# Optimization experiments

Measured on AMD Instinct MI355X. Metric: run time of the kernel, lower is better.

The kernel has to match this reference:

```python
import jax, jax.numpy as jnp
import numpy as np
from jax import lax

N, D = 8, 32            # batch, map_depth
S = 2                   # belief_downsample_factor
HS, WS = 512, 512       # semantic map resolution
H, W = HS // S, WS // S # belief resolution (256, 256)
K = 7                   # motion_kernel_size
KK = K * K
HID = 64                # motion_hidden_size
A = 256                 # action_embedding_size


def _conv(x, w, b, pad, dil=1):
    # x: NCHW, w: OIHW
    y = lax.conv_general_dilated(
        x, w, window_strides=(1, 1), padding=[(pad, pad), (pad, pad)],
        rhs_dilation=(dil, dil), dimension_numbers=('NCHW', 'OIHW', 'NCHW'))
    return y + b[None, :, None, None]


def _unfold_index():
    # Reproduces nn.Unfold([K,K]) applied to ConstantPad2d(K//2, -1)(arange image).
    # Result flattened in (ki*K+kj, i, j) order, matching col2im flatten order.
    pad = K // 2
    img = np.arange(H * W, dtype=np.int64).reshape(H, W)
    imgp = np.pad(img, ((pad, pad), (pad, pad)), constant_values=-1)
    idx = np.empty((K, K, H, W), dtype=np.int64)
    for ki in range(K):
        for kj in range(K):
            idx[ki, kj] = imgp[ki:ki + H, kj:kj + W]
    return idx.reshape(-1)  # (K*K*H*W,)

_IDX = _unfold_index()
_VALID = _IDX >= 0
_IDX_SAFE = np.where(_VALID, _IDX, 0)


def _scatter_logsumexp(src, idx, num_segments):
    # src: (B, M) with -inf marking invalid entries; idx: (M,) shared across B.
    def one(s):
        mx = jax.ops.segment_max(s, idx, num_segments=num_segments)          # (P,)
        g = mx[idx]                                                          # (M,)
        contrib = jnp.where(jnp.isneginf(s), 0.0,
                            jnp.exp(s - jnp.where(jnp.isfinite(g), g, 0.0)))
        sm = jax.ops.segment_sum(contrib, idx, num_segments=num_segments)    # (P,)
        return mx + jnp.log(jnp.where(jnp.isfinite(mx), sm, 1.0))
    return jax.vmap(one)(src)


def setup_inputs() -> dict:
    key = jax.random.key(0)
    ks = jax.random.split(key, 20)
    f32 = jnp.float32
    return {
        'log_belief': jax.random.normal(ks[0], (N, 1, H, W), f32),
        'semantic_map': jax.random.normal(ks[1], (N, D, HS, WS), f32),
        'action': jax.random.normal(ks[2], (N, A), f32),
        # Bottleneck(map_depth -> hidden -> map_depth, dilations [3,1])
        'w_in': jax.random.normal(ks[3], (HID, D, 1, 1), f32) * 0.1,
        'b_in': jnp.zeros((HID,), f32),
        'w_d3': jax.random.normal(ks[4], (HID, HID, 3, 3), f32) * 0.05,
        'b_d3': jnp.zeros((HID,), f32),
        'w_d1': jax.random.normal(ks[5], (HID, HID, 3, 3), f32) * 0.05,
        'b_d1': jnp.zeros((HID,), f32),
        'w_out': jax.random.normal(ks[6], (D, HID, 1, 1), f32) * 0.1,
        'b_out': jnp.zeros((D,), f32),
        # conv1x1: map_depth -> K*K
        'w_k': jax.random.normal(ks[7], (KK, D, 1, 1), f32) * 0.1,
        'b_k': jnp.zeros((KK,), f32),
        # DenseMlpBlock2: A -> hidden -> K*K
        'w_a1': jax.random.normal(ks[8], (A, HID), f32) * 0.05,
        'b_a1': jnp.zeros((HID,), f32),
        'w_a2': jax.random.normal(ks[9], (HID, KK), f32) * 0.05,
        'b_a2': jnp.zeros((KK,), f32),
    }


def reference(log_belief, semantic_map, action,
              w_in, b_in, w_d3, b_d3, w_d1, b_d1, w_out, b_out,
              w_k, b_k, w_a1, b_a1, w_a2, b_a2):
    # Dropout in eval mode -> identity. MaxPool2d(S, stride=S):
    x = lax.reduce_window(semantic_map, -jnp.inf, lax.max,
                          (1, 1, S, S), (1, 1, S, S), 'VALID')  # (N,D,H,W)
    # Bottleneck (conv1x1 -> dilated 3x3 convs -> conv1x1, residual)
    h = jax.nn.relu(_conv(x, w_in, b_in, 0))
    h = jax.nn.relu(_conv(h, w_d3, b_d3, 3, 3))
    h = jax.nn.relu(_conv(h, w_d1, b_d1, 1, 1))
    x2 = x + _conv(h, w_out, b_out, 0)
    # motion kernel logits over K*K taps per pixel
    motion = jax.nn.log_softmax(_conv(x2, w_k, b_k, 0), axis=1)   # (N,KK,H,W)
    lang = jax.nn.log_softmax(
        jax.nn.relu(action @ w_a1 + b_a1) @ w_a2 + b_a2, axis=1)  # (N,KK)
    log_kernel = jax.nn.log_softmax(motion + lang[:, :, None, None], axis=1)
    # propagate_belief: col2im + scatter_logsumexp (C=1, Cin=Cout=1)
    src = (log_belief + log_kernel).reshape(N, -1)                # (N, KK*H*W)
    idx = jnp.asarray(_IDX_SAFE)
    src = jnp.where(jnp.asarray(_VALID)[None, :], src, -jnp.inf)
    new_belief = _scatter_logsumexp(src, idx, H * W)              # (N, H*W)
    return new_belief.reshape(N, 1, H, W)
```

## Files before the change

kernel.cpp:

```cpp
#include <hip/hip_runtime.h>
#include <hip/hip_bf16.h>

typedef __hip_bfloat16 bf16;
typedef __attribute__((ext_vector_type(8)))  short  short8;
typedef __attribute__((ext_vector_type(16))) float  floatx16;

#define HW 65536

__device__ __forceinline__ float b2f(bf16 v){ return __bfloat162float(v); }
__device__ __forceinline__ bf16  f2b(float v){ return __float2bfloat16(v); }
__device__ __forceinline__ unsigned short f2bu(float v){
  union { bf16 h; unsigned short u; } cv; cv.h = __float2bfloat16(v); return cv.u;
}
__device__ __forceinline__ float bu2f(unsigned short u){
  union { unsigned u; float f; } cv; cv.u = ((unsigned)u) << 16; return cv.f;
}

__global__ void prep_w33(const float* __restrict__ w, bf16* __restrict__ wb){
  int i = blockIdx.x*256 + threadIdx.x;
  if (i >= 36864) return;
  int j    = i & 7;
  int gran = i >> 3;
  int oc   = gran & 63;
  int rest = gran >> 6;
  int half = rest & 1;
  int ks   = (rest >> 1) & 3;
  int t    = rest >> 3;
  int e  = ks*16 + half*8 + j;
  int ki = t / 3, kj = t - ki*3;
  wb[i] = f2b(w[(oc*64 + e)*9 + ki*3 + kj]);
}

__global__ void lang_kernel(const float* __restrict__ action,
                            const float* __restrict__ w_a1, const float* __restrict__ b_a1,
                            const float* __restrict__ w_a2, const float* __restrict__ b_a2,
                            float* __restrict__ lang){
  int n = blockIdx.x; int t = threadIdx.x;
  __shared__ float hid[64];
  __shared__ float logits[49];
  __shared__ float lse_sh;
  float acc = b_a1[t];
  for (int a = 0; a < 256; a++) acc += action[n*256+a] * w_a1[a*64+t];
  hid[t] = fmaxf(acc, 0.f);
  __syncthreads();
  if (t < 49){
    float l = b_a2[t];
    for (int j = 0; j < 64; j++) l += hid[j] * w_a2[j*49+t];
    logits[t] = l;
  }
  __syncthreads();
  if (t == 0){
    float m = -1e30f;
    for (int k = 0; k < 49; k++) m = fmaxf(m, logits[k]);
    float s = 0.f;
    for (int k = 0; k < 49; k++) s += __expf(logits[k]-m);
    lse_sh = m + __logf(s);
  }
  __syncthreads();
  if (t < 49) lang[n*49+t] = logits[t] - lse_sh;
}

__global__ __launch_bounds__(256) void pool_in_kernel(
    const float* __restrict__ sm, const float* __restrict__ w_in,
    const float* __restrict__ b_in, float* __restrict__ x, bf16* __restrict__ h1){
  int p = blockIdx.x*256 + threadIdx.x;
  int n = p >> 16; int ij = p & 65535; int i = ij >> 8; int j = ij & 255;
  const float* smn = sm + ((long)n << 23);
  float xv[32];
  #pragma unroll
  for (int d = 0; d < 32; d++){
    long base = ((long)(d*512 + 2*i) << 9) + 2*j;
    float2 p0 = *reinterpret_cast<const float2*>(smn + base);
    float2 p1 = *reinterpret_cast<const float2*>(smn + base + 512);
    xv[d] = fmaxf(fmaxf(p0.x, p0.y), fmaxf(p1.x, p1.y));
  }
  float4* xo = reinterpret_cast<float4*>(x + ((long)p << 5));
  #pragma unroll
  for (int q = 0; q < 8; q++)
    xo[q] = make_float4(xv[4*q], xv[4*q+1], xv[4*q+2], xv[4*q+3]);
  unsigned ow[32];
  #pragma unroll 4
  for (int c = 0; c < 64; c += 2){
    float a0 = b_in[c], a1 = b_in[c+1];
    #pragma unroll
    for (int d = 0; d < 32; d++){
      a0 += xv[d]*w_in[c*32+d];
      a1 += xv[d]*w_in[(c+1)*32+d];
    }
    ow[c>>1] = ((unsigned)f2bu(fmaxf(a1,0.f)) << 16) | f2bu(fmaxf(a0,0.f));
  }
  uint4* ho = reinterpret_cast<uint4*>((char*)h1 + ((long)p << 7));
  #pragma unroll
  for (int q = 0; q < 8; q++)
    ho[q] = make_uint4(ow[4*q], ow[4*q+1], ow[4*q+2], ow[4*q+3]);
}

template<int DIL>
__global__ __launch_bounds__(256) void conv3x3_mfma(
    const bf16* __restrict__ hin, const bf16* __restrict__ wb,
    const float* __restrict__ bias, bf16* __restrict__ hout){
  constexpr int R = 16 + 2*DIL, C = 16 + 2*DIL, NPIX = R*C;
  __shared__ __align__(16) char tile[NPIX*128];
  int b = blockIdx.x;
  int n = b >> 8; int tb = b & 255;
  int i0 = (tb >> 4) << 4, j0 = (tb & 15) << 4;
  int tid = threadIdx.x;
  const bf16* hn = hin + ((long)n << 22);
  for (int s = tid; s < NPIX*8; s += 256){
    int pix = s >> 3, g = s & 7;
    int r = pix / C, c = pix - r*C;
    int gi = i0 - DIL + r, gj = j0 - DIL + c;
    uint4 v = make_uint4(0u,0u,0u,0u);
    if (gi >= 0 && gi < 256 && gj >= 0 && gj < 256)
      v = *reinterpret_cast<const uint4*>(hn + (((long)((gi<<8) + gj)) << 6) + (g<<3));
    *reinterpret_cast<uint4*>(tile + pix*128 + ((g ^ (pix & 7)) << 4)) = v;
  }
  __syncthreads();
  int lane = tid & 63, wv = tid >> 6;
  int mg = wv >> 1, nt = wv & 1;
  int l31 = lane & 31, half = lane >> 5;
  floatx16 acc[4];
  #pragma unroll
  for (int mt = 0; mt < 4; mt++) acc[mt] = (floatx16)(0.0f);
  int prr[4], pcc[4];
  #pragma unroll
  for (int mt = 0; mt < 4; mt++){
    int pidx = (mg*4 + mt)*32 + l31;
    prr[mt] = pidx >> 4; pcc[mt] = pidx & 15;
  }
  const char* wbc = reinterpret_cast<const char*>(wb);
  for (int t = 0; t < 9; t++){
    int ki = t / 3, kj = t - ki*3;
    int pp[4];
    #pragma unroll
    for (int mt = 0; mt < 4; mt++)
      pp[mt] = (prr[mt] + ki*DIL)*C + (pcc[mt] + kj*DIL);
    #pragma unroll
    for (int ks = 0; ks < 4; ks++){
      short8 bfrag = *reinterpret_cast<const short8*>(
          wbc + ((((t*4 + ks)*2 + half)*64 + nt*32 + l31) << 4));
      #pragma unroll
      for (int mt = 0; mt < 4; mt++){
        short8 afrag = *reinterpret_cast<const short8*>(
            tile + pp[mt]*128 + (((ks*2 + half) ^ (pp[mt] & 7)) << 4));
        acc[mt] = __builtin_amdgcn_mfma_f32_32x32x16_bf16(afrag, bfrag, acc[mt], 0, 0, 0);
      }
    }
  }
  float bv = bias[nt*32 + l31];
  bf16* ho = hout + ((long)n << 22);
  #pragma unroll
  for (int mt = 0; mt < 4; mt++){
    #pragma unroll
    for (int reg = 0; reg < 16; reg++){
      int row = (reg & 3) + 8*(reg >> 2) + 4*half;
      int pidx = (mg*4 + mt)*32 + row;
      int pr = pidx >> 4, pc = pidx & 15;
      ho[(((long)(((i0+pr)<<8) + (j0+pc))) << 6) + nt*32 + l31] =
          f2b(fmaxf(acc[mt][reg] + bv, 0.f));
    }
  }
}

__global__ __launch_bounds__(256) void out_motion_kernel(
    const bf16* __restrict__ h3, const float* __restrict__ x,
    const float* __restrict__ w_out, const float* __restrict__ b_out,
    const float* __restrict__ w_k, const float* __restrict__ b_k,
    const float* __restrict__ lang, float* __restrict__ lk){
  int p = blockIdx.x*256 + threadIdx.x;
  int n = p >> 16; int ij = p & 65535;
  float hv[64];
  const uint4* hp = reinterpret_cast<const uint4*>((const char*)h3 + ((long)p << 7));
  #pragma unroll
  for (int q = 0; q < 8; q++){
    uint4 u = hp[q];
    unsigned uu[4] = {u.x, u.y, u.z, u.w};
    #pragma unroll
    for (int k = 0; k < 4; k++){
      hv[q*8 + 2*k]   = bu2f((unsigned short)(uu[k] & 0xffffu));
      hv[q*8 + 2*k+1] = bu2f((unsigned short)(uu[k] >> 16));
    }
  }
  float o[32];
  const float4* xp = reinterpret_cast<const float4*>(x + ((long)p << 5));
  #pragma unroll
  for (int q = 0; q < 8; q++){
    float4 tq = xp[q];
    o[4*q] = tq.x; o[4*q+1] = tq.y; o[4*q+2] = tq.z; o[4*q+3] = tq.w;
  }
  #pragma unroll 4
  for (int d = 0; d < 32; d++){
    float acc = b_out[d];
    #pragma unroll
    for (int e = 0; e < 64; e++) acc += hv[e]*w_out[d*64+e];
    o[d] += acc;
  }
  float lg[49]; float m = -1e30f;
  #pragma unroll 7
  for (int k = 0; k < 49; k++){
    float acc = b_k[k] + lang[n*49+k];
    #pragma unroll
    for (int d = 0; d < 32; d++) acc += o[d]*w_k[k*32+d];
    lg[k] = acc; m = fmaxf(m, acc);
  }
  float s = 0.f;
  #pragma unroll
  for (int k = 0; k < 49; k++) s += __expf(lg[k]-m);
  float lse = m + __logf(s);
  #pragma unroll
  for (int k = 0; k < 49; k++) lk[(long)n*49*HW + (long)k*HW + ij] = lg[k] - lse;
}

__global__ __launch_bounds__(256) void gather_lse_kernel(
    const float* __restrict__ lb, const float* __restrict__ lk, float* __restrict__ out){
  int p = blockIdx.x*256 + threadIdx.x;
  int n = p >> 16; int ij = p & 65535; int i = ij >> 8; int j = ij & 255;
  const float* lkn = lk + (long)n*49*HW;
  float v[49]; float m = -1e30f;
  #pragma unroll
  for (int ki = 0; ki < 7; ki++){
    int h = i + 3 - ki;
    bool hok = (h >= 0 && h < 256);
    #pragma unroll
    for (int kj = 0; kj < 7; kj++){
      int w = j + 3 - kj;
      float val = -1e30f;
      if (hok && w >= 0 && w < 256){
        int q = h*256 + w;
        val = lb[n*HW + q] + lkn[(ki*7+kj)*HW + q];
      }
      v[ki*7+kj] = val; m = fmaxf(m, val);
    }
  }
  float s = 0.f;
  #pragma unroll
  for (int t = 0; t < 49; t++) s += __expf(v[t]-m);
  out[p] = m + __logf(s);
}

extern "C" void kernel_launch(void* const* d_in, const int* in_sizes, int n_in,
                              void* d_out, int out_size, void* d_ws, size_t ws_size,
                              hipStream_t stream) {
  (void)in_sizes; (void)n_in; (void)out_size; (void)ws_size;
  const float* lb    = (const float*)d_in[0];
  const float* sm    = (const float*)d_in[1];
  const float* act   = (const float*)d_in[2];
  const float* w_in  = (const float*)d_in[3];
  const float* b_in  = (const float*)d_in[4];
  const float* w_d3  = (const float*)d_in[5];
  const float* b_d3  = (const float*)d_in[6];
  const float* w_d1  = (const float*)d_in[7];
  const float* b_d1  = (const float*)d_in[8];
  const float* w_out = (const float*)d_in[9];
  const float* b_out = (const float*)d_in[10];
  const float* w_k   = (const float*)d_in[11];
  const float* b_k   = (const float*)d_in[12];
  const float* w_a1  = (const float*)d_in[13];
  const float* b_a1  = (const float*)d_in[14];
  const float* w_a2  = (const float*)d_in[15];
  const float* b_a2  = (const float*)d_in[16];
  float* out = (float*)d_out;

  char* ws = (char*)d_ws;
  float* x    = (float*)(ws + 0);
  bf16*  h1   = (bf16*) (ws + 67108864);
  bf16*  h2   = (bf16*) (ws + 134217728);
  float* lk   = (float*)(ws + 134217728);
  float* lang = (float*)(ws + 236978176);
  bf16*  wb3  = (bf16*) (ws + 236979968);
  bf16*  wb1  = (bf16*) (ws + 237053696);

  prep_w33<<<144, 256, 0, stream>>>(w_d3, wb3);
  prep_w33<<<144, 256, 0, stream>>>(w_d1, wb1);
  lang_kernel<<<8, 64, 0, stream>>>(act, w_a1, b_a1, w_a2, b_a2, lang);

  pool_in_kernel<<<2048, 256, 0, stream>>>(sm, w_in, b_in, x, h1);
  conv3x3_mfma<3><<<2048, 256, 0, stream>>>(h1, wb3, b_d3, h2);
  conv3x3_mfma<1><<<2048, 256, 0, stream>>>(h2, wb1, b_d1, h1);
  out_motion_kernel<<<2048, 256, 0, stream>>>(h1, x, w_out, b_out,
                                              w_k, b_k, lang, lk);
  gather_lse_kernel<<<2048, 256, 0, stream>>>(lb, lk, out);
}
```

Baseline: 719.1 us.

## Store pooled map in bf16, stage per-pixel I/O through LDS, prefetch conv weights

```diff
diff --git a/kernel.cpp b/kernel.cpp
--- a/kernel.cpp
+++ b/kernel.cpp
@@ -14,6 +14,9 @@
 }
 __device__ __forceinline__ float bu2f(unsigned short u){
   union { unsigned u; float f; } cv; cv.u = ((unsigned)u) << 16; return cv.f;
+}
+__device__ __forceinline__ unsigned packbf(float lo, float hi){
+  return ((unsigned)f2bu(hi) << 16) | f2bu(lo);
 }
 
 __global__ void prep_w33(const float* __restrict__ w, bf16* __restrict__ wb){
@@ -62,8 +65,11 @@
 
 __global__ __launch_bounds__(256) void pool_in_kernel(
     const float* __restrict__ sm, const float* __restrict__ w_in,
-    const float* __restrict__ b_in, float* __restrict__ x, bf16* __restrict__ h1){
-  int p = blockIdx.x*256 + threadIdx.x;
+    const float* __restrict__ b_in, bf16* __restrict__ x, bf16* __restrict__ h1){
+  __shared__ unsigned ldh[256*36];
+  __shared__ unsigned ldx[256*20];
+  int tid = threadIdx.x;
+  int p = blockIdx.x*256 + tid;
   int n = p >> 16; int ij = p & 65535; int i = ij >> 8; int j = ij & 255;
   const float* smn = sm + ((long)n << 23);
   float xv[32];
@@ -74,10 +80,12 @@
     float2 p1 = *reinterpret_cast<const float2*>(smn + base + 512);
     xv[d] = fmaxf(fmaxf(p0.x, p0.y), fmaxf(p1.x, p1.y));
   }
-  float4* xo = reinterpret_cast<float4*>(x + ((long)p << 5));
-  #pragma unroll
-  for (int q = 0; q < 8; q++)
-    xo[q] = make_float4(xv[4*q], xv[4*q+1], xv[4*q+2], xv[4*q+3]);
+  #pragma unroll
+  for (int q = 0; q < 4; q++){
+    uint4 v = make_uint4(packbf(xv[8*q],   xv[8*q+1]), packbf(xv[8*q+2], xv[8*q+3]),
+                         packbf(xv[8*q+4], xv[8*q+5]), packbf(xv[8*q+6], xv[8*q+7]));
+    *reinterpret_cast<uint4*>(&ldx[tid*20 + q*4]) = v;
+  }
   unsigned ow[32];
   #pragma unroll 4
   for (int c = 0; c < 64; c += 2){
@@ -87,12 +95,25 @@
       a0 += xv[d]*w_in[c*32+d];
       a1 += xv[d]*w_in[(c+1)*32+d];
     }
-    ow[c>>1] = ((unsigned)f2bu(fmaxf(a1,0.f)) << 16) | f2bu(fmaxf(a0,0.f));
-  }
-  uint4* ho = reinterpret_cast<uint4*>((char*)h1 + ((long)p << 7));
+    ow[c>>1] = packbf(fmaxf(a0,0.f), fmaxf(a1,0.f));
+  }
   #pragma unroll
   for (int q = 0; q < 8; q++)
-    ho[q] = make_uint4(ow[4*q], ow[4*q+1], ow[4*q+2], ow[4*q+3]);
+    *reinterpret_cast<uint4*>(&ldh[tid*36 + q*4]) =
+        make_uint4(ow[4*q], ow[4*q+1], ow[4*q+2], ow[4*q+3]);
+  __syncthreads();
+  uint4* hg = reinterpret_cast<uint4*>(h1 + (((long)blockIdx.x) << 14));
+  #pragma unroll
+  for (int r = 0; r < 8; r++){
+    int s = r*256 + tid; int pix = s >> 3, g = s & 7;
+    hg[s] = *reinterpret_cast<const uint4*>(&ldh[pix*36 + g*4]);
+  }
+  uint4* xg = reinterpret_cast<uint4*>(x + (((long)blockIdx.x) << 13));
+  #pragma unroll
+  for (int r = 0; r < 4; r++){
+    int s = r*256 + tid; int pix = s >> 2, g = s & 3;
+    xg[s] = *reinterpret_cast<const uint4*>(&ldx[pix*20 + g*4]);
+  }
 }
 
 template<int DIL>
@@ -129,7 +150,19 @@
     prr[mt] = pidx >> 4; pcc[mt] = pidx & 15;
   }
   const char* wbc = reinterpret_cast<const char*>(wb);
+  short8 bcur[4];
+  #pragma unroll
+  for (int ks = 0; ks < 4; ks++)
+    bcur[ks] = *reinterpret_cast<const short8*>(
+        wbc + (((ks*2 + half)*64 + nt*32 + l31) << 4));
   for (int t = 0; t < 9; t++){
+    short8 bnext[4];
+    if (t < 8){
+      #pragma unroll
+      for (int ks = 0; ks < 4; ks++)
+        bnext[ks] = *reinterpret_cast<const short8*>(
+            wbc + (((((t+1)*4 + ks)*2 + half)*64 + nt*32 + l31) << 4));
+    }
     int ki = t / 3, kj = t - ki*3;
     int pp[4];
     #pragma unroll
@@ -137,15 +170,15 @@
       pp[mt] = (prr[mt] + ki*DIL)*C + (pcc[mt] + kj*DIL);
     #pragma unroll
     for (int ks = 0; ks < 4; ks++){
-      short8 bfrag = *reinterpret_cast<const short8*>(
-          wbc + ((((t*4 + ks)*2 + half)*64 + nt*32 + l31) << 4));
       #pragma unroll
       for (int mt = 0; mt < 4; mt++){
         short8 afrag = *reinterpret_cast<const short8*>(
             tile + pp[mt]*128 + (((ks*2 + half) ^ (pp[mt] & 7)) << 4));
-        acc[mt] = __builtin_amdgcn_mfma_f32_32x32x16_bf16(afrag, bfrag, acc[mt], 0, 0, 0);
+        acc[mt] = __builtin_amdgcn_mfma_f32_32x32x16_bf16(afrag, bcur[ks], acc[mt], 0, 0, 0);
       }
     }
+    #pragma unroll
+    for (int ks = 0; ks < 4; ks++) bcur[ks] = bnext[ks];
   }
   float bv = bias[nt*32 + l31];
   bf16* ho = hout + ((long)n << 22);
@@ -163,17 +196,32 @@
 }
 
 __global__ __launch_bounds__(256) void out_motion_kernel(
-    const bf16* __restrict__ h3, const float* __restrict__ x,
+    const bf16* __restrict__ h3, const bf16* __restrict__ x,
     const float* __restrict__ w_out, const float* __restrict__ b_out,
     const float* __restrict__ w_k, const float* __restrict__ b_k,
     const float* __restrict__ lang, float* __restrict__ lk){
-  int p = blockIdx.x*256 + threadIdx.x;
+  __shared__ unsigned ldh[256*36];
+  __shared__ unsigned ldx[256*20];
+  int tid = threadIdx.x;
+  const uint4* hg = reinterpret_cast<const uint4*>(h3 + (((long)blockIdx.x) << 14));
+  #pragma unroll
+  for (int r = 0; r < 8; r++){
+    int s = r*256 + tid; int pix = s >> 3, g = s & 7;
+    *reinterpret_cast<uint4*>(&ldh[pix*36 + g*4]) = hg[s];
+  }
+  const uint4* xg = reinterpret_cast<const uint4*>(x + (((long)blockIdx.x) << 13));
+  #pragma unroll
+  for (int r = 0; r < 4; r++){
+    int s = r*256 + tid; int pix = s >> 2, g = s & 3;
+    *reinterpret_cast<uint4*>(&ldx[pix*20 + g*4]) = xg[s];
+  }
+  __syncthreads();
+  int p = blockIdx.x*256 + tid;
   int n = p >> 16; int ij = p & 65535;
   float hv[64];
-  const uint4* hp = reinterpret_cast<const uint4*>((const char*)h3 + ((long)p << 7));
   #pragma unroll
   for (int q = 0; q < 8; q++){
-    uint4 u = hp[q];
+    uint4 u = *reinterpret_cast<const uint4*>(&ldh[tid*36 + q*4]);
     unsigned uu[4] = {u.x, u.y, u.z, u.w};
     #pragma unroll
     for (int k = 0; k < 4; k++){
@@ -182,11 +230,15 @@
     }
   }
   float o[32];
-  const float4* xp = reinterpret_cast<const float4*>(x + ((long)p << 5));
-  #pragma unroll
-  for (int q = 0; q < 8; q++){
-    float4 tq = xp[q];
-    o[4*q] = tq.x; o[4*q+1] = tq.y; o[4*q+2] = tq.z; o[4*q+3] = tq.w;
+  #pragma unroll
+  for (int q = 0; q < 4; q++){
+    uint4 u = *reinterpret_cast<const uint4*>(&ldx[tid*20 + q*4]);
+    unsigned uu[4] = {u.x, u.y, u.z, u.w};
+    #pragma unroll
+    for (int k = 0; k < 4; k++){
+      o[q*8 + 2*k]   = bu2f((unsigned short)(uu[k] & 0xffffu));
+      o[q*8 + 2*k+1] = bu2f((unsigned short)(uu[k] >> 16));
+    }
   }
   #pragma unroll 4
   for (int d = 0; d < 32; d++){
@@ -262,13 +314,13 @@
   float* out = (float*)d_out;
 
   char* ws = (char*)d_ws;
-  float* x    = (float*)(ws + 0);
-  bf16*  h1   = (bf16*) (ws + 67108864);
-  bf16*  h2   = (bf16*) (ws + 134217728);
-  float* lk   = (float*)(ws + 134217728);
-  float* lang = (float*)(ws + 236978176);
-  bf16*  wb3  = (bf16*) (ws + 236979968);
-  bf16*  wb1  = (bf16*) (ws + 237053696);
+  bf16*  x    = (bf16*) (ws + 0);
+  bf16*  h1   = (bf16*) (ws + 33554432);
+  bf16*  h2   = (bf16*) (ws + 100663296);
+  float* lk   = (float*)(ws + 167772160);
+  float* lang = (float*)(ws + 270532608);
+  bf16*  wb3  = (bf16*) (ws + 270534656);
+  bf16*  wb1  = (bf16*) (ws + 270608384);
 
   prep_w33<<<144, 256, 0, stream>>>(w_d3, wb3);
   prep_w33<<<144, 256, 0, stream>>>(w_d1, wb1);
```

After: 720.5 us. About the same (+0.2%).
